# Kernel tuning notes

Hardware: AMD Instinct MI355X
Metric: run time of the kernel (lower is better)

The kernel has to match this reference:

```python
import jax, jax.numpy as jnp
import numpy as np
from jax import lax

T, B, D_IN, H = 512, 128, 512, 512


def setup_inputs() -> dict:
    key = jax.random.key(0)
    k1, k2, k3, k4 = jax.random.split(key, 4)
    ins = jax.random.normal(k1, (T, B, D_IN), dtype=jnp.float32)
    resets = jax.random.bernoulli(k2, 0.05, (T, B))  # episode-boundary reset mask
    carry = jnp.zeros((B, H), dtype=jnp.float32)
    # fused GRU weights: gate order (r, z, n); input denses have no bias in flax GRUCell
    Wi = jax.random.normal(k3, (D_IN, 3 * H), dtype=jnp.float32) * (1.0 / np.sqrt(D_IN))
    Wh = jax.random.normal(k4, (H, 3 * H), dtype=jnp.float32) * (1.0 / np.sqrt(H))
    bh = jnp.zeros((3 * H,), dtype=jnp.float32)
    return {"carry": carry, "ins": ins, "resets": resets, "Wi": Wi, "Wh": Wh, "bh": bh}


def reference(carry, ins, resets, Wi, Wh, bh):
    """ScannedRNN forward: scan a flax GRUCell over time with per-step reset masking.

    Returns (final_carry [B,H], ys [T,B,H]).
    """

    def step(h, xr):
        x, r_mask = xr                       # x: [B,D_in], r_mask: [B]
        h = jnp.where(r_mask[:, None], jnp.zeros_like(h), h)
        gi = x @ Wi                          # [B,3H]  (no input bias in flax GRUCell)
        gh = h @ Wh + bh                     # [B,3H]
        ir, iz, inn = jnp.split(gi, 3, axis=-1)
        hr, hz, hn = jnp.split(gh, 3, axis=-1)
        r = jax.nn.sigmoid(ir + hr)
        z = jax.nn.sigmoid(iz + hz)
        n = jnp.tanh(inn + r * hn)
        new_h = (1.0 - z) * n + z * h
        return new_h, new_h                  # GRUCell returns (new_carry, new_carry)

    final_carry, ys = lax.scan(step, carry, (ins, resets))
    return final_carry, ys
```

## Files before the change

kernel.cpp:

```cpp
#include <hip/hip_runtime.h>

#define T_STEPS 512
#define BATCH   128
#define DIN     512
#define HDIM    512
#define THREEH  1536
#define THREADS 256
#define LDK     520
#define LDG     49
#define NGROUP  4
#define NSLICE  32
#define BC      32
#define HC      16
#define NC      48
#define CNT_STRIDE 16
#define SPIN_MAX (1 << 16)
#define EX_DWORDS (NSLICE * BATCH * HC / 2)
#define NG4 8
#define RW4 16
#define NS4 32
#define EXSLOT 131072
#define FLAGS_OFF  0
#define GBAR_OFF   1088
#define DEC_OFF    1280
#define VD_OFF     2048
#define HS_OFF     3072
#define EX_OFF     4096
#define GI_OFF     (1u<<20)
#define GI_BYTES   201326592ULL

typedef _Float16 half8 __attribute__((ext_vector_type(8)));
typedef _Float16 half4v __attribute__((ext_vector_type(4)));
typedef float    f32x4 __attribute__((ext_vector_type(4)));
typedef unsigned int uint4v __attribute__((ext_vector_type(4)));

__global__ void sniff_kernel(const unsigned int* __restrict__ w,
                             unsigned int* __restrict__ dec) {
  unsigned int local = 0;
  for (int i = threadIdx.x; i < (T_STEPS * BATCH) / 4; i += THREADS) {
    if (w[i] > 1u) local = 1u;
  }
  if (local) atomicOr(dec, 1u);
}

__device__ __forceinline__ void run_gemm(const _Float16* __restrict__ sAa,
                                         const _Float16* __restrict__ sW,
                                         float* __restrict__ sAcc,
                                         int wid, int lane) {
  const int fr = lane & 15;
  const int kb = (lane >> 4) * 8;
  for (int tile = wid; tile < 6; tile += 4) {
    int mi = tile / 3, ni = tile - mi * 3;
    const _Float16* ap = sAa + (mi * 16 + fr) * LDK + kb;
    const _Float16* bp = sW  + (ni * 16 + fr) * LDK + kb;
    f32x4 acc = {0.f, 0.f, 0.f, 0.f};
#pragma unroll
    for (int kk = 0; kk < DIN / 32; ++kk)
      acc = __builtin_amdgcn_mfma_f32_16x16x32_f16(
          *(const half8*)(ap + kk * 32),
          *(const half8*)(bp + kk * 32), acc, 0, 0, 0);
    int crow = mi * 16 + (lane >> 4) * 4;
    int ccol = ni * 16 + fr;
#pragma unroll
    for (int j = 0; j < 4; ++j) sAcc[(crow + j) * LDG + ccol] = acc[j];
  }
}

__global__ __launch_bounds__(THREADS, 1)
void gru_kernel_v1(const float* __restrict__ carry,
                   const float* __restrict__ ins,
                   const void*  __restrict__ resets_raw,
                   const float* __restrict__ Wi,
                   const float* __restrict__ Wh,
                   const float* __restrict__ bh,
                   float* __restrict__ out,
                   unsigned int* __restrict__ cnt,
                   unsigned int* __restrict__ ex0,
                   unsigned int* __restrict__ ex1,
                   const unsigned int* __restrict__ dec)
{
  __shared__ alignas(16) _Float16 sWi[NC * LDK];
  __shared__ alignas(16) _Float16 sWh[NC * LDK];
  __shared__ alignas(16) _Float16 sA [BC * LDK];
  __shared__ float sGi[BC * LDG];
  __shared__ float sGh[BC * LDG];
  __shared__ float sBh[NC];
  __shared__ int   sRst[BC];

  const int tid  = threadIdx.x;
  const int bid  = blockIdx.x;
  const int g    = bid & (NGROUP - 1);
  const int p    = bid >> 2;
  const int row0 = g * BC;
  const int col0 = p * HC;

  float* carryOut = out;
  float* ys = out + BATCH * HDIM;

  const unsigned int isBool = *dec;
  const unsigned char* r8  = (const unsigned char*)resets_raw;
  const int*           r32 = (const int*)resets_raw;

  unsigned int* ex[2] = { ex0, ex1 };
  unsigned int* myCnt = cnt + g * CNT_STRIDE;

  for (int idx = tid; idx < DIN * NC; idx += THREADS) {
    int k  = idx / NC;
    int ci = idx - k * NC;
    int gcol = (ci >> 4) * HDIM + col0 + (ci & 15);
    sWi[ci * LDK + k] = (_Float16)Wi[k * THREEH + gcol];
    sWh[ci * LDK + k] = (_Float16)Wh[k * THREEH + gcol];
  }
  if (tid < NC) {
    int gcol = (tid >> 4) * HDIM + col0 + (tid & 15);
    sBh[tid] = bh[gcol];
  }

  float hreg[2];
  {
    int idx = tid * 2;
    int b0 = idx >> 4, c0 = idx & 15;
    hreg[0] = carry[(size_t)(row0 + b0) * HDIM + col0 + c0];
    hreg[1] = carry[(size_t)(row0 + b0) * HDIM + col0 + c0 + 1];
  }

  const int wid  = tid >> 6;
  const int lane = tid & 63;

  auto stageRst = [&](int t) {
    if (tid < BC) {
      int off = t * BATCH + row0 + tid;
      sRst[tid] = isBool ? (int)r8[off] : r32[off];
    }
  };
  auto stageX = [&](int t) {
    const float4* src = (const float4*)(ins + (size_t)(t * BATCH + row0) * DIN);
    for (int i = tid; i < BC * (DIN / 4); i += THREADS) {
      int r = i >> 7, c4 = i & 127;
      float4 v = src[(size_t)r * 128 + c4];
      half4v hv = {(_Float16)v.x, (_Float16)v.y, (_Float16)v.z, (_Float16)v.w};
      *(half4v*)&sA[r * LDK + c4 * 4] = hv;
    }
  };

  stageRst(0);
  stageX(0);
  __syncthreads();
  run_gemm(sA, sWi, sGi, wid, lane);
  __syncthreads();
  {
    const float4* src = (const float4*)(carry + (size_t)row0 * HDIM);
    for (int i = tid; i < BC * (HDIM / 4); i += THREADS) {
      int r = i >> 7, c4 = i & 127;
      float4 v = src[(size_t)r * 128 + c4];
      float m = sRst[r] ? 0.f : 1.f;
      half4v hv = {(_Float16)(v.x*m), (_Float16)(v.y*m),
                   (_Float16)(v.z*m), (_Float16)(v.w*m)};
      *(half4v*)&sA[r * LDK + c4 * 4] = hv;
    }
  }
  __syncthreads();

  for (int t = 0; t < T_STEPS; ++t) {
    if (t > 0) {
      {
        const unsigned int target = 32u * (unsigned)t;
        unsigned int fv;
        for (int it = 0; it < SPIN_MAX; ++it) {
          asm volatile("global_load_dword %0, %1, off sc0 sc1\n\t"
                       "s_waitcnt vmcnt(0)"
                       : "=v"(fv) : "v"(myCnt) : "memory");
          if (fv >= target) break;
          __builtin_amdgcn_s_sleep(1);
        }
      }
      {
        const unsigned int* exsrc = ex[(t - 1) & 1];
        uint4v vv[8];
#pragma unroll
        for (int j = 0; j < 8; ++j) {
          int i = tid + THREADS * j;
          int p_ = i >> 6, b_ = (i >> 1) & 31, hw = (i & 1) << 2;
          const unsigned int* sp = exsrc + p_ * 1024 + (row0 + b_) * 8 + hw;
          asm volatile("global_load_dwordx4 %0, %1, off sc0 sc1"
                       : "=&v"(vv[j]) : "v"(sp) : "memory");
        }
        asm volatile("s_waitcnt vmcnt(0)" ::: "memory");
        __builtin_amdgcn_sched_barrier(0);
#pragma unroll
        for (int j = 0; j < 8; ++j) {
          int i = tid + THREADS * j;
          int p_ = i >> 6, b_ = (i >> 1) & 31, hw = (i & 1) << 3;
          half8 hv = *reinterpret_cast<half8*>(&vv[j]);
          half8 z = {(_Float16)0, (_Float16)0, (_Float16)0, (_Float16)0,
                     (_Float16)0, (_Float16)0, (_Float16)0, (_Float16)0};
          hv = sRst[b_] ? z : hv;
          *(half8*)&sA[b_ * LDK + p_ * 16 + hw] = hv;
        }
      }
      __syncthreads();
    }

    run_gemm(sA, sWh, sGh, wid, lane);
    __syncthreads();

    {
#pragma unroll
      for (int e = 0; e < 2; ++e) {
        int idx = tid * 2 + e;
        int b = idx >> 4, cj = idx & 15;
        float gir = sGi[b * LDG + cj];
        float giz = sGi[b * LDG + 16 + cj];
        float gin = sGi[b * LDG + 32 + cj];
        float ghr = sGh[b * LDG + cj]      + sBh[cj];
        float ghz = sGh[b * LDG + 16 + cj] + sBh[16 + cj];
        float ghn = sGh[b * LDG + 32 + cj] + sBh[32 + cj];
        float r = 1.f / (1.f + __expf(-(gir + ghr)));
        float z = 1.f / (1.f + __expf(-(giz + ghz)));
        float n = tanhf(gin + r * ghn);
        float hp = sRst[b] ? 0.f : hreg[e];
        hreg[e] = (1.f - z) * n + z * hp;
      }
      union { _Float16 h[2]; unsigned int u; } pk;
      pk.h[0] = (_Float16)hreg[0];
      pk.h[1] = (_Float16)hreg[1];
      unsigned int* dst = ex[t & 1] + p * 1024 + (row0 + (tid >> 3)) * 8 + (tid & 7);
      asm volatile("global_store_dword %0, %1, off sc0 sc1"
                   :: "v"(dst), "v"(pk.u) : "memory");
      int b0 = (tid * 2) >> 4, c0 = (tid * 2) & 15;
      float2 yv = make_float2(hreg[0], hreg[1]);
      *(float2*)&ys[((size_t)t * BATCH + row0 + b0) * HDIM + col0 + c0] = yv;
      if (t == T_STEPS - 1)
        *(float2*)&carryOut[(size_t)(row0 + b0) * HDIM + col0 + c0] = yv;
    }
    asm volatile("s_waitcnt vmcnt(0)" ::: "memory");
    __syncthreads();
    if (tid == 0) atomicAdd(myCnt, 1u);

    if (t < T_STEPS - 1) {
      stageRst(t + 1);
      stageX(t + 1);
      __syncthreads();
      run_gemm(sA, sWi, sGi, wid, lane);
      __syncthreads();
    }
  }
}

__global__ __launch_bounds__(256, 1)
void gi_prepass2(const float* __restrict__ ins,
                 const float* __restrict__ Wi,
                 _Float16* __restrict__ gis)
{
  __shared__ alignas(16) _Float16 sWiT[48 * LDK];
  __shared__ alignas(16) _Float16 sX[32 * LDK];

  const int tid = threadIdx.x;
  const int bid = blockIdx.x;
  const int n   = bid >> 3;
  const int mg  = bid & 7;
  const int wid = tid >> 6;
  const int lane = tid & 63;
  const int fr = lane & 15;
  const int kb = (lane >> 4) * 8;

  for (int idx = tid; idx < 48 * DIN; idx += 256) {
    int ci = idx % 48, k = idx / 48;
    int gcol = (ci >> 4) * HDIM + n * 16 + (ci & 15);
    sWiT[ci * LDK + k] = (_Float16)Wi[(size_t)k * THREEH + gcol];
  }

  float4 va[16];
  auto LOADS = [&](int ch) {
    const float4* src = (const float4*)(ins + (size_t)(mg * 8192 + ch * 32) * DIN);
#pragma unroll
    for (int j = 0; j < 16; ++j) va[j] = src[tid + 256 * j];
  };
  auto WRITE = [&]() {
#pragma unroll
    for (int j = 0; j < 16; ++j) {
      int i = tid + 256 * j;
      int r = i >> 7, c4 = i & 127;
      float4 v = va[j];
      half4v hv = {(_Float16)v.x, (_Float16)v.y, (_Float16)v.z, (_Float16)v.w};
      *(half4v*)&sX[r * LDK + c4 * 4] = hv;
    }
  };

  LOADS(0);
  for (int ch = 0; ch < 256; ++ch) {
    WRITE();
    __syncthreads();
    if (ch + 1 < 256) LOADS(ch + 1);

    const int m0 = mg * 8192 + ch * 32;
    const int tt = m0 >> 7;
    const int bb0 = m0 & 127;
    for (int tile = wid; tile < 6; tile += 4) {
      int mi = tile / 3, ni = tile - mi * 3;
      const _Float16* ap = sX   + (mi * 16 + fr) * LDK + kb;
      const _Float16* bp = sWiT + (ni * 16 + fr) * LDK + kb;
      f32x4 acc = {0.f, 0.f, 0.f, 0.f};
#pragma unroll
      for (int kk = 0; kk < DIN / 32; ++kk)
        acc = __builtin_amdgcn_mfma_f32_16x16x32_f16(
            *(const half8*)(ap + kk * 32),
            *(const half8*)(bp + kk * 32), acc, 0, 0, 0);
      int gr = mi * 16 + ((lane >> 4) << 2);
      int col = n * 16 + fr;
      size_t base = ((size_t)(tt * 3 + ni) * BATCH) * HDIM + col;
#pragma unroll
      for (int j = 0; j < 4; ++j)
        gis[base + (size_t)(bb0 + gr + j) * HDIM] = (_Float16)acc[j];
    }
    __syncthreads();
  }
}

__device__ __forceinline__ void gridbar(unsigned int* ctr, int tid) {
  __syncthreads();
  if (tid == 0) {
    atomicAdd(ctr, 1u);
    unsigned int v;
    for (int it = 0; it < SPIN_MAX; ++it) {
      asm volatile("global_load_dword %0, %1, off sc0 sc1\n\t"
                   "s_waitcnt vmcnt(0)" : "=v"(v) : "v"(ctr) : "memory");
      if (v >= 256u) break;
      __builtin_amdgcn_s_sleep(1);
    }
  }
  __syncthreads();
}

__global__ __launch_bounds__(256, 1)
void gru_kernel_v4(const float* __restrict__ carry,
                   const void*  __restrict__ resets_raw,
                   const float* __restrict__ Wh,
                   const float* __restrict__ bh,
                   float* __restrict__ out,
                   unsigned int* __restrict__ wsb,
                   const _Float16* __restrict__ gis,
                   const unsigned int* __restrict__ dec)
{
  __shared__ alignas(16) _Float16 sWh[NC * LDK];
  __shared__ alignas(16) _Float16 sA [RW4 * LDK];
  __shared__ float sGh[RW4 * LDG];
  __shared__ float sBh[NC];
  __shared__ int   sRst[RW4];
  __shared__ int   sFast;

  const int tid  = threadIdx.x;
  const int bid  = blockIdx.x;
  const int g    = bid & 7;
  const int p    = bid >> 3;
  const int row0 = g * RW4;
  const int col0 = p * HC;

  unsigned int* flags = wsb + (FLAGS_OFF / 4) ;
  unsigned int* gbars = wsb + (GBAR_OFF / 4);
  unsigned int* vd    = wsb + (VD_OFF / 4);
  unsigned int* hs    = wsb + (HS_OFF / 4);
  char*         exb   = (char*)wsb + EX_OFF;

  float* carryOut = out;
  float* ys = out + BATCH * HDIM;

  const unsigned int isBool = *dec;
  const unsigned char* r8  = (const unsigned char*)resets_raw;
  const int*           r32 = (const int*)resets_raw;

  bool ok1 = true, ok2 = true;
  {
    unsigned int PAT1 = 0xC0DE0000u | (unsigned)bid;
    unsigned int PAT2 = 0xFACE0000u | (unsigned)bid;
    if (tid == 0) {
      unsigned int* hp = hs + bid;
      asm volatile("global_store_dword %0, %1, off sc0\n\t"
                   "s_waitcnt vmcnt(0)" :: "v"(hp), "v"(PAT1) : "memory");
    }
    gridbar(gbars + 0 * 16, tid);
    if (tid < 32) {
      int peer = g + 8 * tid;
      unsigned int v;
      const unsigned int* hp = hs + peer;
      asm volatile("global_load_dword %0, %1, off sc0\n\t"
                   "s_waitcnt vmcnt(0)" : "=v"(v) : "v"(hp) : "memory");
      ok1 = (v == (0xC0DE0000u | (unsigned)peer));
    }
    gridbar(gbars + 1 * 16, tid);
    if (tid == 0) {
      unsigned int* hp = hs + bid;
      asm volatile("global_store_dword %0, %1, off sc0\n\t"
                   "s_waitcnt vmcnt(0)" :: "v"(hp), "v"(PAT2) : "memory");
    }
    gridbar(gbars + 2 * 16, tid);
    if (tid < 32) {
      int peer = g + 8 * tid;
      unsigned int v;
      const unsigned int* hp = hs + peer;
      asm volatile("global_load_dword %0, %1, off sc0\n\t"
                   "s_waitcnt vmcnt(0)" : "=v"(v) : "v"(hp) : "memory");
      ok2 = (v == (0xFACE0000u | (unsigned)peer));
    }
    bool myok = (tid < 32) ? (ok1 && ok2) : true;
    bool wgok = __all(myok);
    if (tid == 0) {
      unsigned int vv = wgok ? 1u : 0u;
      unsigned int* vp = vd + bid;
      asm volatile("global_store_dword %0, %1, off sc0 sc1\n\t"
                   "s_waitcnt vmcnt(0)" :: "v"(vp), "v"(vv) : "memory");
    }
    gridbar(gbars + 3 * 16, tid);
    bool fin = true;
    if (tid < 32) {
      int peer = g + 8 * tid;
      unsigned int v;
      const unsigned int* vp = vd + peer;
      asm volatile("global_load_dword %0, %1, off sc0 sc1\n\t"
                   "s_waitcnt vmcnt(0)" : "=v"(v) : "v"(vp) : "memory");
      fin = (v == 1u);
    }
    bool unan = __all((tid < 32) ? fin : true);
    if (tid == 0) sFast = unan ? 1 : 0;
    __syncthreads();
  }
  const int fast = sFast;

  if (tid == 0) {
    unsigned int* fp = flags + (g * 32 + p);
    unsigned int zz = 0u;
    if (fast) {
      asm volatile("global_store_dword %0, %1, off sc0\n\t"
                   "s_waitcnt vmcnt(0)" :: "v"(fp), "v"(zz) : "memory");
    } else {
      asm volatile("global_store_dword %0, %1, off sc0 sc1\n\t"
                   "s_waitcnt vmcnt(0)" :: "v"(fp), "v"(zz) : "memory");
    }
  }
  gridbar(gbars + 4 * 16, tid);

  for (int idx = tid; idx < DIN * NC; idx += THREADS) {
    int k  = idx / NC;
    int ci = idx - k * NC;
    int gcol = (ci >> 4) * HDIM + col0 + (ci & 15);
    sWh[ci * LDK + k] = (_Float16)Wh[k * THREEH + gcol];
  }
  if (tid < NC) {
    int gcol = (tid >> 4) * HDIM + col0 + (tid & 15);
    sBh[tid] = bh[gcol];
  }

  const int gb = tid >> 4;
  const int gc = tid & 15;
  float hreg = carry[(size_t)(row0 + gb) * HDIM + col0 + gc];

  const int wid  = tid >> 6;
  const int lane = tid & 63;
  const int fr   = lane & 15;
  const int kb   = (lane >> 4) * 8;

  if (tid < RW4) {
    int off = row0 + tid;
    sRst[tid] = isBool ? (int)r8[off] : r32[off];
  }
  __syncthreads();
  {
    const float4* src = (const float4*)(carry + (size_t)row0 * HDIM);
    for (int i = tid; i < RW4 * (HDIM / 4); i += THREADS) {
      int r = i >> 7, c4 = i & 127;
      float4 v = src[(size_t)r * 128 + c4];
      float m = sRst[r] ? 0.f : 1.f;
      half4v hv = {(_Float16)(v.x*m), (_Float16)(v.y*m),
                   (_Float16)(v.z*m), (_Float16)(v.w*m)};
      *(half4v*)&sA[r * LDK + c4 * 4] = hv;
    }
  }

  const unsigned short* gisu = (const unsigned short*)gis;

  for (int t = 0; t < T_STEPS; ++t) {
    unsigned short gu0, gu1, gu2;
    {
      size_t base = ((size_t)(t * 3) * BATCH + row0 + gb) * HDIM + col0 + gc;
      gu0 = gisu[base];
      gu1 = gisu[base + (size_t)BATCH * HDIM];
      gu2 = gisu[base + 2 * (size_t)BATCH * HDIM];
    }
    if (t > 0 && tid < RW4) {
      int off = t * BATCH + row0 + tid;
      sRst[tid] = isBool ? (int)r8[off] : r32[off];
    }
    if (t > 0) {
      bool done = false;
      const unsigned int* fp = flags + (g * 32 + (tid & 31));
      for (int it = 0; it < SPIN_MAX && !done; ++it) {
        unsigned int fv = 0xFFFFFFFFu;
        if (tid < 32) {
          if (fast) {
            asm volatile("global_load_dword %0, %1, off sc0\n\t"
                         "s_waitcnt vmcnt(0)" : "=v"(fv) : "v"(fp) : "memory");
          } else {
            asm volatile("global_load_dword %0, %1, off sc0 sc1\n\t"
                         "s_waitcnt vmcnt(0)" : "=v"(fv) : "v"(fp) : "memory");
          }
        }
        done = __all((tid < 32) ? (fv >= (unsigned)t) : true);
        if (!done) __builtin_amdgcn_s_sleep(1);
      }
    }
    __syncthreads();

    if (t > 0) {
      const char* src = exb + ((t - 1) & 1) * EXSLOT + g * 16384
                      + (tid >> 4) * 1024 + (tid & 15) * 64;
      uint4v v0, v1, v2, v3;
      if (fast) {
        asm volatile("global_load_dwordx4 %0, %4, off sc0\n\t"
                     "global_load_dwordx4 %1, %4, off offset:16 sc0\n\t"
                     "global_load_dwordx4 %2, %4, off offset:32 sc0\n\t"
                     "global_load_dwordx4 %3, %4, off offset:48 sc0\n\t"
                     "s_waitcnt vmcnt(0)"
                     : "=&v"(v0), "=&v"(v1), "=&v"(v2), "=&v"(v3)
                     : "v"(src) : "memory");
      } else {
        asm volatile("global_load_dwordx4 %0, %4, off sc0 sc1\n\t"
                     "global_load_dwordx4 %1, %4, off offset:16 sc0 sc1\n\t"
                     "global_load_dwordx4 %2, %4, off offset:32 sc0 sc1\n\t"
                     "global_load_dwordx4 %3, %4, off offset:48 sc0 sc1\n\t"
                     "s_waitcnt vmcnt(0)"
                     : "=&v"(v0), "=&v"(v1), "=&v"(v2), "=&v"(v3)
                     : "v"(src) : "memory");
      }
      __builtin_amdgcn_sched_barrier(0);
      int r = tid >> 4, c0 = (tid & 15) * 32;
      half8 h0 = *reinterpret_cast<half8*>(&v0);
      half8 h1 = *reinterpret_cast<half8*>(&v1);
      half8 h2 = *reinterpret_cast<half8*>(&v2);
      half8 h3 = *reinterpret_cast<half8*>(&v3);
      half8 z = {(_Float16)0, (_Float16)0, (_Float16)0, (_Float16)0,
                 (_Float16)0, (_Float16)0, (_Float16)0, (_Float16)0};
      if (sRst[r]) { h0 = z; h1 = z; h2 = z; h3 = z; }
      *(half8*)&sA[r * LDK + c0 +  0] = h0;
      *(half8*)&sA[r * LDK + c0 +  8] = h1;
      *(half8*)&sA[r * LDK + c0 + 16] = h2;
      *(half8*)&sA[r * LDK + c0 + 24] = h3;
      __syncthreads();
    }

    if (wid < 3) {
      const int ni = wid;
      const _Float16* ap = sA  + fr * LDK + kb;
      const _Float16* bp = sWh + (ni * 16 + fr) * LDK + kb;
      f32x4 a0 = {0.f, 0.f, 0.f, 0.f}, a1 = {0.f, 0.f, 0.f, 0.f};
#pragma unroll
      for (int kk = 0; kk < DIN / 32; kk += 2) {
        a0 = __builtin_amdgcn_mfma_f32_16x16x32_f16(
            *(const half8*)(ap + kk * 32), *(const half8*)(bp + kk * 32), a0, 0, 0, 0);
        a1 = __builtin_amdgcn_mfma_f32_16x16x32_f16(
            *(const half8*)(ap + (kk + 1) * 32), *(const half8*)(bp + (kk + 1) * 32), a1, 0, 0, 0);
      }
      a0 += a1;
      int crow = (lane >> 4) * 4;
      int ccol = ni * 16 + fr;
#pragma unroll
      for (int j = 0; j < 4; ++j) sGh[(crow + j) * LDG + ccol] = a0[j];
    }
    __syncthreads();

    {
      union { unsigned short u; _Float16 h; } c0_, c1_, c2_;
      c0_.u = gu0; c1_.u = gu1; c2_.u = gu2;
      float gir = (float)c0_.h;
      float giz = (float)c1_.h;
      float gin = (float)c2_.h;
      float ghr = sGh[gb * LDG + gc]      + sBh[gc];
      float ghz = sGh[gb * LDG + 16 + gc] + sBh[16 + gc];
      float ghn = sGh[gb * LDG + 32 + gc] + sBh[32 + gc];
      float r = 1.f / (1.f + __expf(-(gir + ghr)));
      float z = 1.f / (1.f + __expf(-(giz + ghz)));
      float n = tanhf(gin + r * ghn);
      float hp = sRst[gb] ? 0.f : hreg;
      hreg = (1.f - z) * n + z * hp;

      union { _Float16 h; unsigned short u; } pk;
      pk.h = (_Float16)hreg;
      unsigned int pv = (unsigned int)pk.u;
      unsigned short* dst = (unsigned short*)
        (exb + (t & 1) * EXSLOT + g * 16384 + gb * 1024 + (col0 + gc) * 2);
      if (fast) {
        asm volatile("global_store_short %0, %1, off sc0"
                     :: "v"(dst), "v"(pv) : "memory");
      } else {
        asm volatile("global_store_short %0, %1, off sc0 sc1"
                     :: "v"(dst), "v"(pv) : "memory");
      }
    }
    asm volatile("s_waitcnt vmcnt(0)" ::: "memory");
    __syncthreads();
    if (tid == 0) {
      unsigned int* fp = flags + (g * 32 + p);
      unsigned int val = (unsigned)(t + 1);
      if (fast) {
        asm volatile("global_store_dword %0, %1, off sc0"
                     :: "v"(fp), "v"(val) : "memory");
      } else {
        asm volatile("global_store_dword %0, %1, off sc0 sc1"
                     :: "v"(fp), "v"(val) : "memory");
      }
    }
    {
      ys[((size_t)t * BATCH + row0 + gb) * HDIM + col0 + gc] = hreg;
      if (t == T_STEPS - 1)
        carryOut[(size_t)(row0 + gb) * HDIM + col0 + gc] = hreg;
    }
  }

  __builtin_amdgcn_fence(__ATOMIC_RELEASE, "agent");
}

extern "C" void kernel_launch(void* const* d_in, const int* in_sizes, int n_in,
                              void* d_out, int out_size, void* d_ws, size_t ws_size,
                              hipStream_t stream) {
  const float* carry  = (const float*)d_in[0];
  const float* ins    = (const float*)d_in[1];
  const void*  resets = (const void*)d_in[2];
  const float* Wi     = (const float*)d_in[3];
  const float* Wh     = (const float*)d_in[4];
  const float* bh     = (const float*)d_in[5];
  float* out = (float*)d_out;

  unsigned int* wsb  = (unsigned int*)d_ws;
  unsigned int* dec  = (unsigned int*)((char*)d_ws + DEC_OFF);
  unsigned int* ex0  = (unsigned int*)((char*)d_ws + EX_OFF);
  unsigned int* ex1  = ex0 + EX_DWORDS;
  _Float16*     gis  = (_Float16*)((char*)d_ws + GI_OFF);

  (void)hipMemsetAsync(d_ws, 0, 4096, stream);

  sniff_kernel<<<dim3(1), dim3(THREADS), 0, stream>>>(
      (const unsigned int*)resets, dec);

  const bool bigWs = ws_size >= (size_t)GI_OFF + GI_BYTES;

  if (bigWs) {
    gi_prepass2<<<dim3(256), dim3(256), 0, stream>>>(ins, Wi, gis);
    void* args[] = { (void*)&carry, (void*)&resets, (void*)&Wh, (void*)&bh,
                     (void*)&out, (void*)&wsb, (void*)&gis, (void*)&dec };
    (void)hipLaunchCooperativeKernel((const void*)gru_kernel_v4,
                                     dim3(256), dim3(256),
                                     args, 0, stream);
  } else {
    void* args[] = { (void*)&carry, (void*)&ins, (void*)&resets, (void*)&Wi,
                     (void*)&Wh, (void*)&bh, (void*)&out, (void*)&wsb,
                     (void*)&ex0, (void*)&ex1, (void*)&dec };
    (void)hipLaunchCooperativeKernel((const void*)gru_kernel_v1,
                                     dim3(NGROUP * NSLICE), dim3(THREADS),
                                     args, 0, stream);
  }
}
```

Baseline: 2.140 ms.

## Fuse input projection into persistent GRU kernel with producer warps overlapping recurrence

Drops the separate gi prepass kernel that wrote a large fp16 input-projection buffer to global memory. The persistent cooperative kernel now uses 512 threads: four waves run the recurrent step, and the extra waves prefetch x two steps ahead and compute x@Wi one step ahead into a small shared ring buffer. Per-wave flags replace the per-block flag and block barrier, reset masks are preloaded as bitmasks, and the handshake now uses a nonce. This removes the prepass time and its global traffic. In exchange it doubles the threads per block, needs more shared memory for Wi, and puts input-GEMM work inside the latency-critical step loop.

```diff
diff --git a/kernel.cpp b/kernel.cpp
--- a/kernel.cpp
+++ b/kernel.cpp
@@ -5,29 +5,29 @@
 #define DIN     512
 #define HDIM    512
 #define THREEH  1536
-#define THREADS 256
 #define LDK     520
 #define LDG     49
+#define SPIN_MAX (1 << 16)
+#define HS_SPIN  512
+#define THREADS 256
 #define NGROUP  4
 #define NSLICE  32
 #define BC      32
 #define HC      16
 #define NC      48
 #define CNT_STRIDE 16
-#define SPIN_MAX (1 << 16)
 #define EX_DWORDS (NSLICE * BATCH * HC / 2)
-#define NG4 8
-#define RW4 16
-#define NS4 32
-#define EXSLOT 131072
+#define THREADS7 512
+#define RW 16
+#define EXSLOT7 131072
 #define FLAGS_OFF  0
-#define GBAR_OFF   1088
-#define DEC_OFF    1280
-#define VD_OFF     2048
-#define HS_OFF     3072
-#define EX_OFF     4096
-#define GI_OFF     (1u<<20)
-#define GI_BYTES   201326592ULL
+#define GBAR_OFF   4096
+#define NONCE_OFF  4608
+#define DEC_OFF    4736
+#define VD_OFF     5120
+#define HS_OFF     6144
+#define MEMSET_BYTES 8192
+#define EX_OFF     8192
 
 typedef _Float16 half8 __attribute__((ext_vector_type(8)));
 typedef _Float16 half4v __attribute__((ext_vector_type(4)));
@@ -37,7 +37,7 @@
 __global__ void sniff_kernel(const unsigned int* __restrict__ w,
                              unsigned int* __restrict__ dec) {
   unsigned int local = 0;
-  for (int i = threadIdx.x; i < (T_STEPS * BATCH) / 4; i += THREADS) {
+  for (int i = threadIdx.x; i < (T_STEPS * BATCH) / 4; i += 256) {
     if (w[i] > 1u) local = 1u;
   }
   if (local) atomicOr(dec, 1u);
@@ -247,77 +247,7 @@
   }
 }
 
-__global__ __launch_bounds__(256, 1)
-void gi_prepass2(const float* __restrict__ ins,
-                 const float* __restrict__ Wi,
-                 _Float16* __restrict__ gis)
-{
-  __shared__ alignas(16) _Float16 sWiT[48 * LDK];
-  __shared__ alignas(16) _Float16 sX[32 * LDK];
-
-  const int tid = threadIdx.x;
-  const int bid = blockIdx.x;
-  const int n   = bid >> 3;
-  const int mg  = bid & 7;
-  const int wid = tid >> 6;
-  const int lane = tid & 63;
-  const int fr = lane & 15;
-  const int kb = (lane >> 4) * 8;
-
-  for (int idx = tid; idx < 48 * DIN; idx += 256) {
-    int ci = idx % 48, k = idx / 48;
-    int gcol = (ci >> 4) * HDIM + n * 16 + (ci & 15);
-    sWiT[ci * LDK + k] = (_Float16)Wi[(size_t)k * THREEH + gcol];
-  }
-
-  float4 va[16];
-  auto LOADS = [&](int ch) {
-    const float4* src = (const float4*)(ins + (size_t)(mg * 8192 + ch * 32) * DIN);
-#pragma unroll
-    for (int j = 0; j < 16; ++j) va[j] = src[tid + 256 * j];
-  };
-  auto WRITE = [&]() {
-#pragma unroll
-    for (int j = 0; j < 16; ++j) {
-      int i = tid + 256 * j;
-      int r = i >> 7, c4 = i & 127;
-      float4 v = va[j];
-      half4v hv = {(_Float16)v.x, (_Float16)v.y, (_Float16)v.z, (_Float16)v.w};
-      *(half4v*)&sX[r * LDK + c4 * 4] = hv;
-    }
-  };
-
-  LOADS(0);
-  for (int ch = 0; ch < 256; ++ch) {
-    WRITE();
-    __syncthreads();
-    if (ch + 1 < 256) LOADS(ch + 1);
-
-    const int m0 = mg * 8192 + ch * 32;
-    const int tt = m0 >> 7;
-    const int bb0 = m0 & 127;
-    for (int tile = wid; tile < 6; tile += 4) {
-      int mi = tile / 3, ni = tile - mi * 3;
-      const _Float16* ap = sX   + (mi * 16 + fr) * LDK + kb;
-      const _Float16* bp = sWiT + (ni * 16 + fr) * LDK + kb;
-      f32x4 acc = {0.f, 0.f, 0.f, 0.f};
-#pragma unroll
-      for (int kk = 0; kk < DIN / 32; ++kk)
-        acc = __builtin_amdgcn_mfma_f32_16x16x32_f16(
-            *(const half8*)(ap + kk * 32),
-            *(const half8*)(bp + kk * 32), acc, 0, 0, 0);
-      int gr = mi * 16 + ((lane >> 4) << 2);
-      int col = n * 16 + fr;
-      size_t base = ((size_t)(tt * 3 + ni) * BATCH) * HDIM + col;
-#pragma unroll
-      for (int j = 0; j < 4; ++j)
-        gis[base + (size_t)(bb0 + gr + j) * HDIM] = (_Float16)acc[j];
-    }
-    __syncthreads();
-  }
-}
-
-__device__ __forceinline__ void gridbar(unsigned int* ctr, int tid) {
+__device__ __forceinline__ void gridbar7(unsigned int* ctr, int tid) {
   __syncthreads();
   if (tid == 0) {
     atomicAdd(ctr, 1u);
@@ -332,35 +262,41 @@
   __syncthreads();
 }
 
-__global__ __launch_bounds__(256, 1)
-void gru_kernel_v4(const float* __restrict__ carry,
+__global__ __launch_bounds__(THREADS7, 1)
+void gru_kernel_v7(const float* __restrict__ carry,
+                   const float* __restrict__ ins,
                    const void*  __restrict__ resets_raw,
+                   const float* __restrict__ Wi,
                    const float* __restrict__ Wh,
                    const float* __restrict__ bh,
                    float* __restrict__ out,
                    unsigned int* __restrict__ wsb,
-                   const _Float16* __restrict__ gis,
                    const unsigned int* __restrict__ dec)
 {
   __shared__ alignas(16) _Float16 sWh[NC * LDK];
-  __shared__ alignas(16) _Float16 sA [RW4 * LDK];
-  __shared__ float sGh[RW4 * LDG];
+  __shared__ alignas(16) _Float16 sWi[NC * LDK];
+  __shared__ alignas(16) _Float16 sA [RW * LDK];
+  __shared__ alignas(16) _Float16 xbuf[2][RW * LDK];
+  __shared__ alignas(16) _Float16 sGi3[3 * 3 * 16 * 16];
+  __shared__ float sGh[RW * LDG];
   __shared__ float sBh[NC];
-  __shared__ int   sRst[RW4];
+  __shared__ unsigned short sRstB[T_STEPS];
   __shared__ int   sFast;
+  __shared__ unsigned int sNonce;
 
   const int tid  = threadIdx.x;
   const int bid  = blockIdx.x;
   const int g    = bid & 7;
   const int p    = bid >> 3;
-  const int row0 = g * RW4;
+  const int row0 = g * RW;
   const int col0 = p * HC;
 
-  unsigned int* flags = wsb + (FLAGS_OFF / 4) ;
-  unsigned int* gbars = wsb + (GBAR_OFF / 4);
-  unsigned int* vd    = wsb + (VD_OFF / 4);
-  unsigned int* hs    = wsb + (HS_OFF / 4);
-  char*         exb   = (char*)wsb + EX_OFF;
+  unsigned int* flags    = wsb + (FLAGS_OFF / 4);
+  unsigned int* gbars    = wsb + (GBAR_OFF / 4);
+  unsigned int* nonceArr = wsb + (NONCE_OFF / 4);
+  unsigned int* vd       = wsb + (VD_OFF / 4);
+  unsigned int* hs       = wsb + (HS_OFF / 4);
+  char*         exb      = (char*)wsb + EX_OFF;
 
   float* carryOut = out;
   float* ys = out + BATCH * HDIM;
@@ -368,192 +304,253 @@
   const unsigned int isBool = *dec;
   const unsigned char* r8  = (const unsigned char*)resets_raw;
   const int*           r32 = (const int*)resets_raw;
-
-  bool ok1 = true, ok2 = true;
-  {
-    unsigned int PAT1 = 0xC0DE0000u | (unsigned)bid;
-    unsigned int PAT2 = 0xFACE0000u | (unsigned)bid;
-    if (tid == 0) {
-      unsigned int* hp = hs + bid;
-      asm volatile("global_store_dword %0, %1, off sc0\n\t"
-                   "s_waitcnt vmcnt(0)" :: "v"(hp), "v"(PAT1) : "memory");
-    }
-    gridbar(gbars + 0 * 16, tid);
-    if (tid < 32) {
-      int peer = g + 8 * tid;
-      unsigned int v;
-      const unsigned int* hp = hs + peer;
-      asm volatile("global_load_dword %0, %1, off sc0\n\t"
-                   "s_waitcnt vmcnt(0)" : "=v"(v) : "v"(hp) : "memory");
-      ok1 = (v == (0xC0DE0000u | (unsigned)peer));
-    }
-    gridbar(gbars + 1 * 16, tid);
-    if (tid == 0) {
-      unsigned int* hp = hs + bid;
-      asm volatile("global_store_dword %0, %1, off sc0\n\t"
-                   "s_waitcnt vmcnt(0)" :: "v"(hp), "v"(PAT2) : "memory");
-    }
-    gridbar(gbars + 2 * 16, tid);
-    if (tid < 32) {
-      int peer = g + 8 * tid;
-      unsigned int v;
-      const unsigned int* hp = hs + peer;
-      asm volatile("global_load_dword %0, %1, off sc0\n\t"
-                   "s_waitcnt vmcnt(0)" : "=v"(v) : "v"(hp) : "memory");
-      ok2 = (v == (0xFACE0000u | (unsigned)peer));
-    }
-    bool myok = (tid < 32) ? (ok1 && ok2) : true;
-    bool wgok = __all(myok);
-    if (tid == 0) {
-      unsigned int vv = wgok ? 1u : 0u;
-      unsigned int* vp = vd + bid;
-      asm volatile("global_store_dword %0, %1, off sc0 sc1\n\t"
-                   "s_waitcnt vmcnt(0)" :: "v"(vp), "v"(vv) : "memory");
-    }
-    gridbar(gbars + 3 * 16, tid);
-    bool fin = true;
-    if (tid < 32) {
-      int peer = g + 8 * tid;
-      unsigned int v;
-      const unsigned int* vp = vd + peer;
-      asm volatile("global_load_dword %0, %1, off sc0 sc1\n\t"
-                   "s_waitcnt vmcnt(0)" : "=v"(v) : "v"(vp) : "memory");
-      fin = (v == 1u);
-    }
-    bool unan = __all((tid < 32) ? fin : true);
-    if (tid == 0) sFast = unan ? 1 : 0;
-    __syncthreads();
-  }
-  const int fast = sFast;
-
-  if (tid == 0) {
-    unsigned int* fp = flags + (g * 32 + p);
-    unsigned int zz = 0u;
-    if (fast) {
-      asm volatile("global_store_dword %0, %1, off sc0\n\t"
-                   "s_waitcnt vmcnt(0)" :: "v"(fp), "v"(zz) : "memory");
-    } else {
-      asm volatile("global_store_dword %0, %1, off sc0 sc1\n\t"
-                   "s_waitcnt vmcnt(0)" :: "v"(fp), "v"(zz) : "memory");
-    }
-  }
-  gridbar(gbars + 4 * 16, tid);
-
-  for (int idx = tid; idx < DIN * NC; idx += THREADS) {
-    int k  = idx / NC;
-    int ci = idx - k * NC;
-    int gcol = (ci >> 4) * HDIM + col0 + (ci & 15);
-    sWh[ci * LDK + k] = (_Float16)Wh[k * THREEH + gcol];
-  }
-  if (tid < NC) {
-    int gcol = (tid >> 4) * HDIM + col0 + (tid & 15);
-    sBh[tid] = bh[gcol];
-  }
-
-  const int gb = tid >> 4;
-  const int gc = tid & 15;
-  float hreg = carry[(size_t)(row0 + gb) * HDIM + col0 + gc];
 
   const int wid  = tid >> 6;
   const int lane = tid & 63;
   const int fr   = lane & 15;
   const int kb   = (lane >> 4) * 8;
-
-  if (tid < RW4) {
-    int off = row0 + tid;
-    sRst[tid] = isBool ? (int)r8[off] : r32[off];
+  const int gb   = tid >> 4;
+  const int gc   = tid & 15;
+
+  for (int idx = tid; idx < DIN * NC; idx += THREADS7) {
+    int k  = idx / NC;
+    int ci = idx - k * NC;
+    int gcol = (ci >> 4) * HDIM + col0 + (ci & 15);
+    sWh[ci * LDK + k] = (_Float16)Wh[(size_t)k * THREEH + gcol];
+    sWi[ci * LDK + k] = (_Float16)Wi[(size_t)k * THREEH + gcol];
+  }
+  if (tid < NC) {
+    int gcol = (tid >> 4) * HDIM + col0 + (tid & 15);
+    sBh[tid] = bh[gcol];
+  }
+  if (tid < T_STEPS) {
+    unsigned int m = 0;
+#pragma unroll
+    for (int r = 0; r < RW; ++r) {
+      int off = tid * BATCH + row0 + r;
+      int v = isBool ? (int)r8[off] : r32[off];
+      m |= (v ? 1u : 0u) << r;
+    }
+    sRstB[tid] = (unsigned short)m;
+  }
+  float hreg = 0.f;
+  if (tid < 256) hreg = carry[(size_t)(row0 + gb) * HDIM + col0 + gc];
+
+  if (p == 0 && tid == 0) {
+    unsigned long long tv = __builtin_amdgcn_s_memrealtime();
+    unsigned int nv = (unsigned int)(tv ^ (tv >> 32));
+    if (nv == 0) nv = 0x5A5A5A5Au;
+    asm volatile("global_store_dword %0, %1, off sc0 sc1\n\t"
+                 "s_waitcnt vmcnt(0)" :: "v"(nonceArr + g), "v"(nv) : "memory");
+  }
+  gridbar7(gbars + 0 * 16, tid);
+  if (tid == 0) {
+    unsigned int nv;
+    asm volatile("global_load_dword %0, %1, off sc0 sc1\n\t"
+                 "s_waitcnt vmcnt(0)" : "=v"(nv) : "v"(nonceArr + g) : "memory");
+    sNonce = nv;
   }
   __syncthreads();
+  const unsigned int nonce = sNonce;
+
+  bool okAll = true;
+  for (int r = 0; r < 2; ++r) {
+    if (tid == 0) {
+      unsigned int tok = nonce ^ ((unsigned)p << 8) ^ ((unsigned)(r + 1) << 20);
+      asm volatile("global_store_dword %0, %1, off sc0\n\t"
+                   "s_waitcnt vmcnt(0)" :: "v"(hs + bid), "v"(tok) : "memory");
+    }
+    __syncthreads();
+    if (tid < 32) {
+      unsigned int expv = nonce ^ ((unsigned)tid << 8) ^ ((unsigned)(r + 1) << 20);
+      const unsigned int* hp = hs + (g + 8 * tid);
+      bool got = false;
+      for (int it = 0; it < HS_SPIN && !got; ++it) {
+        unsigned int v;
+        asm volatile("global_load_dword %0, %1, off sc0\n\t"
+                     "s_waitcnt vmcnt(0)" : "=v"(v) : "v"(hp) : "memory");
+        got = (v == expv);
+      }
+      okAll = okAll && got;
+    }
+    gridbar7(gbars + (1 + r) * 16, tid);
+  }
   {
-    const float4* src = (const float4*)(carry + (size_t)row0 * HDIM);
-    for (int i = tid; i < RW4 * (HDIM / 4); i += THREADS) {
+    bool wgok = __all((tid < 32) ? okAll : true);
+    if (tid == 0) {
+      unsigned int vv = wgok ? 1u : 0u;
+      asm volatile("global_store_dword %0, %1, off sc0 sc1\n\t"
+                   "s_waitcnt vmcnt(0)" :: "v"(vd + bid), "v"(vv) : "memory");
+    }
+    gridbar7(gbars + 3 * 16, tid);
+    bool fin = true;
+    if (tid < 32) {
+      unsigned int v;
+      asm volatile("global_load_dword %0, %1, off sc0 sc1\n\t"
+                   "s_waitcnt vmcnt(0)" : "=v"(v) : "v"(vd + (g + 8 * tid)) : "memory");
+      fin = (v == 1u);
+    }
+    bool unan = __all((tid < 32) ? fin : true);
+    if (tid == 0) sFast = unan ? 1 : 0;
+    __syncthreads();
+  }
+  const int fast = sFast;
+
+  for (int s = 0; s < 2; ++s) {
+    const float4* src = (const float4*)(ins + (size_t)(s * BATCH + row0) * DIN);
+    for (int i = tid; i < RW * 128; i += THREADS7) {
       int r = i >> 7, c4 = i & 127;
       float4 v = src[(size_t)r * 128 + c4];
-      float m = sRst[r] ? 0.f : 1.f;
-      half4v hv = {(_Float16)(v.x*m), (_Float16)(v.y*m),
-                   (_Float16)(v.z*m), (_Float16)(v.w*m)};
-      *(half4v*)&sA[r * LDK + c4 * 4] = hv;
-    }
-  }
-
-  const unsigned short* gisu = (const unsigned short*)gis;
+      half4v hv = {(_Float16)v.x, (_Float16)v.y, (_Float16)v.z, (_Float16)v.w};
+      *(half4v*)&xbuf[s][r * LDK + c4 * 4] = hv;
+    }
+  }
+  __syncthreads();
+  if (wid >= 4 && wid < 7) {
+    int ni = wid - 4;
+    const _Float16* ap = &xbuf[0][fr * LDK + kb];
+    const _Float16* bp = sWi + (ni * 16 + fr) * LDK + kb;
+    f32x4 a0 = {0.f, 0.f, 0.f, 0.f}, a1 = {0.f, 0.f, 0.f, 0.f};
+#pragma unroll
+    for (int kk = 0; kk < 16; kk += 2) {
+      a0 = __builtin_amdgcn_mfma_f32_16x16x32_f16(
+          *(const half8*)(ap + kk * 32), *(const half8*)(bp + kk * 32), a0, 0, 0, 0);
+      a1 = __builtin_amdgcn_mfma_f32_16x16x32_f16(
+          *(const half8*)(ap + (kk + 1) * 32), *(const half8*)(bp + (kk + 1) * 32), a1, 0, 0, 0);
+    }
+    a0 += a1;
+    int crow = (lane >> 4) * 4;
+#pragma unroll
+    for (int j = 0; j < 4; ++j)
+      sGi3[0 * 768 + ni * 256 + (crow + j) * 16 + fr] = (_Float16)a0[j];
+  }
+
+  float4 xv[8];
+  const int xi = (tid & 255);
 
   for (int t = 0; t < T_STEPS; ++t) {
-    unsigned short gu0, gu1, gu2;
-    {
-      size_t base = ((size_t)(t * 3) * BATCH + row0 + gb) * HDIM + col0 + gc;
-      gu0 = gisu[base];
-      gu1 = gisu[base + (size_t)BATCH * HDIM];
-      gu2 = gisu[base + 2 * (size_t)BATCH * HDIM];
-    }
-    if (t > 0 && tid < RW4) {
-      int off = t * BATCH + row0 + tid;
-      sRst[tid] = isBool ? (int)r8[off] : r32[off];
-    }
-    if (t > 0) {
-      bool done = false;
-      const unsigned int* fp = flags + (g * 32 + (tid & 31));
-      for (int it = 0; it < SPIN_MAX && !done; ++it) {
-        unsigned int fv = 0xFFFFFFFFu;
-        if (tid < 32) {
+    const int slot  = t & 1;
+    const int gslot = t % 3;
+
+    if (wid < 4) {
+      if (t > 0 && tid < 64) {
+        const unsigned int* f1 = flags + g * 128 + tid;
+        const unsigned int* f2 = flags + g * 128 + 64 + tid;
+        bool done = false;
+        for (int it = 0; it < SPIN_MAX && !done; ++it) {
+          unsigned int a, b;
           if (fast) {
-            asm volatile("global_load_dword %0, %1, off sc0\n\t"
-                         "s_waitcnt vmcnt(0)" : "=v"(fv) : "v"(fp) : "memory");
+            asm volatile("global_load_dword %0, %2, off sc0\n\t"
+                         "global_load_dword %1, %3, off sc0\n\t"
+                         "s_waitcnt vmcnt(0)"
+                         : "=&v"(a), "=&v"(b) : "v"(f1), "v"(f2) : "memory");
           } else {
-            asm volatile("global_load_dword %0, %1, off sc0 sc1\n\t"
-                         "s_waitcnt vmcnt(0)" : "=v"(fv) : "v"(fp) : "memory");
+            asm volatile("global_load_dword %0, %2, off sc0 sc1\n\t"
+                         "global_load_dword %1, %3, off sc0 sc1\n\t"
+                         "s_waitcnt vmcnt(0)"
+                         : "=&v"(a), "=&v"(b) : "v"(f1), "v"(f2) : "memory");
           }
-        }
-        done = __all((tid < 32) ? (fv >= (unsigned)t) : true);
-        if (!done) __builtin_amdgcn_s_sleep(1);
+          done = __all(a >= (unsigned)t && b >= (unsigned)t);
+          if (!done && it > 64) __builtin_amdgcn_s_sleep(1);
+        }
+      }
+    } else {
+      if (t + 2 < T_STEPS) {
+        const float4* src = (const float4*)(ins + (size_t)((t + 2) * BATCH + row0) * DIN);
+#pragma unroll
+        for (int j = 0; j < 8; ++j) {
+          int i = xi + 256 * j;
+          xv[j] = src[(size_t)(i >> 7) * 128 + (i & 127)];
+        }
+      }
+      if (t + 1 < T_STEPS && wid < 7) {
+        int ni = wid - 4;
+        const _Float16* ap = &xbuf[(t + 1) & 1][fr * LDK + kb];
+        const _Float16* bp = sWi + (ni * 16 + fr) * LDK + kb;
+        f32x4 a0 = {0.f, 0.f, 0.f, 0.f}, a1 = {0.f, 0.f, 0.f, 0.f};
+#pragma unroll
+        for (int kk = 0; kk < 16; kk += 2) {
+          a0 = __builtin_amdgcn_mfma_f32_16x16x32_f16(
+              *(const half8*)(ap + kk * 32), *(const half8*)(bp + kk * 32), a0, 0, 0, 0);
+          a1 = __builtin_amdgcn_mfma_f32_16x16x32_f16(
+              *(const half8*)(ap + (kk + 1) * 32), *(const half8*)(bp + (kk + 1) * 32), a1, 0, 0, 0);
+        }
+        a0 += a1;
+        int crow = (lane >> 4) * 4;
+#pragma unroll
+        for (int j = 0; j < 4; ++j)
+          sGi3[((t + 1) % 3) * 768 + ni * 256 + (crow + j) * 16 + fr] = (_Float16)a0[j];
       }
     }
     __syncthreads();
 
-    if (t > 0) {
-      const char* src = exb + ((t - 1) & 1) * EXSLOT + g * 16384
-                      + (tid >> 4) * 1024 + (tid & 15) * 64;
-      uint4v v0, v1, v2, v3;
-      if (fast) {
-        asm volatile("global_load_dwordx4 %0, %4, off sc0\n\t"
-                     "global_load_dwordx4 %1, %4, off offset:16 sc0\n\t"
-                     "global_load_dwordx4 %2, %4, off offset:32 sc0\n\t"
-                     "global_load_dwordx4 %3, %4, off offset:48 sc0\n\t"
-                     "s_waitcnt vmcnt(0)"
-                     : "=&v"(v0), "=&v"(v1), "=&v"(v2), "=&v"(v3)
-                     : "v"(src) : "memory");
+    if (tid < 256) {
+      if (t == 0) {
+        const float4* src = (const float4*)(carry + (size_t)row0 * HDIM);
+        const unsigned int rm = sRstB[0];
+        for (int i = tid; i < RW * 128; i += 256) {
+          int r = i >> 7, c4 = i & 127;
+          float4 v = src[(size_t)r * 128 + c4];
+          float m = ((rm >> r) & 1u) ? 0.f : 1.f;
+          half4v hv = {(_Float16)(v.x*m), (_Float16)(v.y*m),
+                       (_Float16)(v.z*m), (_Float16)(v.w*m)};
+          *(half4v*)&sA[r * LDK + c4 * 4] = hv;
+        }
       } else {
-        asm volatile("global_load_dwordx4 %0, %4, off sc0 sc1\n\t"
-                     "global_load_dwordx4 %1, %4, off offset:16 sc0 sc1\n\t"
-                     "global_load_dwordx4 %2, %4, off offset:32 sc0 sc1\n\t"
-                     "global_load_dwordx4 %3, %4, off offset:48 sc0 sc1\n\t"
-                     "s_waitcnt vmcnt(0)"
-                     : "=&v"(v0), "=&v"(v1), "=&v"(v2), "=&v"(v3)
-                     : "v"(src) : "memory");
-      }
+        const char* src = exb + (slot ^ 1) * EXSLOT7 + g * 16384
+                        + (tid >> 4) * 1024 + (tid & 15) * 64;
+        uint4v v0, v1, v2, v3;
+        if (fast) {
+          asm volatile("global_load_dwordx4 %0, %4, off sc0\n\t"
+                       "global_load_dwordx4 %1, %4, off offset:16 sc0\n\t"
+                       "global_load_dwordx4 %2, %4, off offset:32 sc0\n\t"
+                       "global_load_dwordx4 %3, %4, off offset:48 sc0\n\t"
+                       "s_waitcnt vmcnt(0)"
+                       : "=&v"(v0), "=&v"(v1), "=&v"(v2), "=&v"(v3)
+                       : "v"(src) : "memory");
+        } else {
+          asm volatile("global_load_dwordx4 %0, %4, off sc0 sc1\n\t"
+                       "global_load_dwordx4 %1, %4, off offset:16 sc0 sc1\n\t"
+                       "global_load_dwordx4 %2, %4, off offset:32 sc0 sc1\n\t"
+                       "global_load_dwordx4 %3, %4, off offset:48 sc0 sc1\n\t"
+                       "s_waitcnt vmcnt(0)"
+                       : "=&v"(v0), "=&v"(v1), "=&v"(v2), "=&v"(v3)
+                       : "v"(src) : "memory");
+        }
+        __builtin_amdgcn_sched_barrier(0);
+        int r = tid >> 4, c0 = (tid & 15) * 32;
+        half8 h0 = *reinterpret_cast<half8*>(&v0);
+        half8 h1 = *reinterpret_cast<half8*>(&v1);
+        half8 h2 = *reinterpret_cast<half8*>(&v2);
+        half8 h3 = *reinterpret_cast<half8*>(&v3);
+        half8 z = {(_Float16)0, (_Float16)0, (_Float16)0, (_Float16)0,
+                   (_Float16)0, (_Float16)0, (_Float16)0, (_Float16)0};
+        if ((sRstB[t] >> r) & 1u) { h0 = z; h1 = z; h2 = z; h3 = z; }
+        *(half8*)&sA[r * LDK + c0 +  0] = h0;
+        *(half8*)&sA[r * LDK + c0 +  8] = h1;
+        *(half8*)&sA[r * LDK + c0 + 16] = h2;
+        *(half8*)&sA[r * LDK + c0 + 24] = h3;
+      }
+    } else if (t + 2 < T_STEPS) {
+      asm volatile("s_waitcnt vmcnt(0)" ::: "memory");
       __builtin_amdgcn_sched_barrier(0);
-      int r = tid >> 4, c0 = (tid & 15) * 32;
-      half8 h0 = *reinterpret_cast<half8*>(&v0);
-      half8 h1 = *reinterpret_cast<half8*>(&v1);
-      half8 h2 = *reinterpret_cast<half8*>(&v2);
-      half8 h3 = *reinterpret_cast<half8*>(&v3);
-      half8 z = {(_Float16)0, (_Float16)0, (_Float16)0, (_Float16)0,
-                 (_Float16)0, (_Float16)0, (_Float16)0, (_Float16)0};
-      if (sRst[r]) { h0 = z; h1 = z; h2 = z; h3 = z; }
-      *(half8*)&sA[r * LDK + c0 +  0] = h0;
-      *(half8*)&sA[r * LDK + c0 +  8] = h1;
-      *(half8*)&sA[r * LDK + c0 + 16] = h2;
-      *(half8*)&sA[r * LDK + c0 + 24] = h3;
-      __syncthreads();
-    }
+#pragma unroll
+      for (int j = 0; j < 8; ++j) {
+        int i = xi + 256 * j;
+        int r = i >> 7, c4 = i & 127;
+        float4 v = xv[j];
+        half4v hv = {(_Float16)v.x, (_Float16)v.y, (_Float16)v.z, (_Float16)v.w};
+        *(half4v*)&xbuf[t & 1][r * LDK + c4 * 4] = hv;
+      }
+    }
+    __syncthreads();
 
     if (wid < 3) {
-      const int ni = wid;
       const _Float16* ap = sA  + fr * LDK + kb;
-      const _Float16* bp = sWh + (ni * 16 + fr) * LDK + kb;
+      const _Float16* bp = sWh + (wid * 16 + fr) * LDK + kb;
       f32x4 a0 = {0.f, 0.f, 0.f, 0.f}, a1 = {0.f, 0.f, 0.f, 0.f};
 #pragma unroll
-      for (int kk = 0; kk < DIN / 32; kk += 2) {
+      for (int kk = 0; kk < 16; kk += 2) {
         a0 = __builtin_amdgcn_mfma_f32_16x16x32_f16(
             *(const half8*)(ap + kk * 32), *(const half8*)(bp + kk * 32), a0, 0, 0, 0);
         a1 = __builtin_amdgcn_mfma_f32_16x16x32_f16(
@@ -561,54 +558,40 @@
       }
       a0 += a1;
       int crow = (lane >> 4) * 4;
-      int ccol = ni * 16 + fr;
+      int ccol = wid * 16 + fr;
 #pragma unroll
       for (int j = 0; j < 4; ++j) sGh[(crow + j) * LDG + ccol] = a0[j];
     }
     __syncthreads();
 
-    {
-      union { unsigned short u; _Float16 h; } c0_, c1_, c2_;
-      c0_.u = gu0; c1_.u = gu1; c2_.u = gu2;
-      float gir = (float)c0_.h;
-      float giz = (float)c1_.h;
-      float gin = (float)c2_.h;
+    if (tid < 256) {
+      float gir = (float)sGi3[gslot * 768 + 0 * 256 + gb * 16 + gc];
+      float giz = (float)sGi3[gslot * 768 + 1 * 256 + gb * 16 + gc];
+      float gin = (float)sGi3[gslot * 768 + 2 * 256 + gb * 16 + gc];
       float ghr = sGh[gb * LDG + gc]      + sBh[gc];
       float ghz = sGh[gb * LDG + 16 + gc] + sBh[16 + gc];
       float ghn = sGh[gb * LDG + 32 + gc] + sBh[32 + gc];
       float r = 1.f / (1.f + __expf(-(gir + ghr)));
       float z = 1.f / (1.f + __expf(-(giz + ghz)));
       float n = tanhf(gin + r * ghn);
-      float hp = sRst[gb] ? 0.f : hreg;
+      float hp = ((sRstB[t] >> gb) & 1u) ? 0.f : hreg;
       hreg = (1.f - z) * n + z * hp;
 
-      union { _Float16 h; unsigned short u; } pk;
-      pk.h = (_Float16)hreg;
-      unsigned int pv = (unsigned int)pk.u;
-      unsigned short* dst = (unsigned short*)
-        (exb + (t & 1) * EXSLOT + g * 16384 + gb * 1024 + (col0 + gc) * 2);
-      if (fast) {
-        asm volatile("global_store_short %0, %1, off sc0"
-                     :: "v"(dst), "v"(pv) : "memory");
-      } else {
-        asm volatile("global_store_short %0, %1, off sc0 sc1"
-                     :: "v"(dst), "v"(pv) : "memory");
-      }
-    }
-    asm volatile("s_waitcnt vmcnt(0)" ::: "memory");
-    __syncthreads();
-    if (tid == 0) {
-      unsigned int* fp = flags + (g * 32 + p);
-      unsigned int val = (unsigned)(t + 1);
-      if (fast) {
-        asm volatile("global_store_dword %0, %1, off sc0"
-                     :: "v"(fp), "v"(val) : "memory");
-      } else {
-        asm volatile("global_store_dword %0, %1, off sc0 sc1"
-                     :: "v"(fp), "v"(val) : "memory");
-      }
-    }
-    {
+      if (t < T_STEPS - 1) {
+        union { _Float16 h; unsigned short u; } pk;
+        pk.h = (_Float16)hreg;
+        unsigned int pv = (unsigned int)pk.u;
+        char* dst = exb + slot * EXSLOT7 + g * 16384 + gb * 1024 + (col0 + gc) * 2;
+        if (fast) asm volatile("global_store_short %0, %1, off sc0" :: "v"(dst), "v"(pv) : "memory");
+        else      asm volatile("global_store_short %0, %1, off sc0 sc1" :: "v"(dst), "v"(pv) : "memory");
+        asm volatile("s_waitcnt vmcnt(0)" ::: "memory");
+        if (lane == 0) {
+          unsigned int* fp = flags + g * 128 + p * 4 + wid;
+          unsigned int val = (unsigned)(t + 1);
+          if (fast) asm volatile("global_store_dword %0, %1, off sc0" :: "v"(fp), "v"(val) : "memory");
+          else      asm volatile("global_store_dword %0, %1, off sc0 sc1" :: "v"(fp), "v"(val) : "memory");
+        }
+      }
       ys[((size_t)t * BATCH + row0 + gb) * HDIM + col0 + gc] = hreg;
       if (t == T_STEPS - 1)
         carryOut[(size_t)(row0 + gb) * HDIM + col0 + gc] = hreg;
@@ -633,21 +616,20 @@
   unsigned int* dec  = (unsigned int*)((char*)d_ws + DEC_OFF);
   unsigned int* ex0  = (unsigned int*)((char*)d_ws + EX_OFF);
   unsigned int* ex1  = ex0 + EX_DWORDS;
-  _Float16*     gis  = (_Float16*)((char*)d_ws + GI_OFF);
-
-  (void)hipMemsetAsync(d_ws, 0, 4096, stream);
-
-  sniff_kernel<<<dim3(1), dim3(THREADS), 0, stream>>>(
+
+  (void)hipMemsetAsync(d_ws, 0, MEMSET_BYTES, stream);
+
+  sniff_kernel<<<dim3(1), dim3(256), 0, stream>>>(
       (const unsigned int*)resets, dec);
 
-  const bool bigWs = ws_size >= (size_t)GI_OFF + GI_BYTES;
-
-  if (bigWs) {
-    gi_prepass2<<<dim3(256), dim3(256), 0, stream>>>(ins, Wi, gis);
-    void* args[] = { (void*)&carry, (void*)&resets, (void*)&Wh, (void*)&bh,
-                     (void*)&out, (void*)&wsb, (void*)&gis, (void*)&dec };
-    (void)hipLaunchCooperativeKernel((const void*)gru_kernel_v4,
-                                     dim3(256), dim3(256),
+  const bool okWs = ws_size >= (size_t)EX_OFF + 2 * EXSLOT7;
+
+  if (okWs) {
+    void* args[] = { (void*)&carry, (void*)&ins, (void*)&resets, (void*)&Wi,
+                     (void*)&Wh, (void*)&bh, (void*)&out, (void*)&wsb,
+                     (void*)&dec };
+    (void)hipLaunchCooperativeKernel((const void*)gru_kernel_v7,
+                                     dim3(256), dim3(THREADS7),
                                      args, 0, stream);
   } else {
     void* args[] = { (void*)&carry, (void*)&ins, (void*)&resets, (void*)&Wi,
```

Result: slower. 2.689 ms (+25.7%).
